# Performance work log

Measured on AMD Instinct MI355X. Metric: run time of the kernel, lower is better.

The kernel has to match this reference:

```python
import jax, jax.numpy as jnp
import numpy as np

C, H, W = 16, 16, 16      # observation_shape
T, B = 128, 128           # rollout steps x num envs
HID = 512                 # LSTM / fc hidden
ZD = 8                    # z_dim (options)
AD = 7                    # action_dim
FE = 128                  # lo_feat dim


def setup_inputs() -> dict:
    key = jax.random.key(0)
    ks = jax.random.split(key, 16)
    def rn(k, shape, s=0.02):
        return jax.random.normal(k, shape, jnp.float32) * s
    return dict(
        x=jax.random.normal(ks[0], (T * B, C, H, W), jnp.float32),
        done=jax.random.randint(ks[1], (T * B,), 0, 2, jnp.int32),
        z=jax.random.randint(ks[2], (T * B,), 0, ZD, jnp.int32),
        action=jax.random.randint(ks[3], (T * B,), 0, AD, jnp.int32),
        h0=jnp.zeros((1, B, HID), jnp.float32),
        c0=jnp.zeros((1, B, HID), jnp.float32),
        conv1_w=rn(ks[4], (C, C, 5, 5)), conv1_b=jnp.zeros((C,), jnp.float32),
        conv2_w=rn(ks[5], (C, C, 3, 3)), conv2_b=jnp.zeros((C,), jnp.float32),
        conv3_w=rn(ks[6], (C, C, 3, 3)), conv3_b=jnp.zeros((C,), jnp.float32),
        fc1_w=rn(ks[7], (HID, C * H * W)), fc1_b=jnp.zeros((HID,), jnp.float32),
        fc2_w=rn(ks[8], (HID, HID)), fc2_b=jnp.zeros((HID,), jnp.float32),
        w_ih=rn(ks[9], (4 * HID, HID)), w_hh=rn(ks[10], (4 * HID, HID)),
        b_ih=jnp.zeros((4 * HID,), jnp.float32), b_hh=jnp.zeros((4 * HID,), jnp.float32),
        lofeat_w=rn(ks[11], (FE, HID + ZD)), lofeat_b=jnp.zeros((FE,), jnp.float32),
        actor_w=rn(ks[12], (AD, FE)), actor_b=jnp.zeros((AD,), jnp.float32),
        critic_w=rn(ks[13], (1, FE)), critic_b=jnp.zeros((1,), jnp.float32),
    )


def _leaky(v):
    return jnp.where(v > 0, v, 0.01 * v)  # nn.LeakyReLU default slope


def reference(x, done, z, action, h0, c0,
              conv1_w, conv1_b, conv2_w, conv2_b, conv3_w, conv3_b,
              fc1_w, fc1_b, fc2_w, fc2_b,
              w_ih, w_hh, b_ih, b_hh,
              lofeat_w, lofeat_b, actor_w, actor_b, critic_w, critic_b):
    dn = ('NCHW', 'OIHW', 'NCHW')
    h = x
    for wgt, bias in ((conv1_w, conv1_b), (conv2_w, conv2_b), (conv3_w, conv3_b)):
        h = _leaky(jax.lax.conv_general_dilated(h, wgt, (1, 1), 'SAME',
                                                dimension_numbers=dn)
                   + bias[None, :, None, None])
    h = h.reshape(h.shape[0], -1)                 # [TB, C*H*W]
    h = _leaky(h @ fc1_w.T + fc1_b)
    h = _leaky(h @ fc2_w.T + fc2_b)               # [TB, 512]

    hs = h.reshape(T, B, HID)                     # env_first=False layout
    ds = done.astype(h.dtype).reshape(T, B)

    def step(carry, inp):
        hc, cc = carry
        xt, dt = inp
        m = (1.0 - dt)[:, None]                   # done-based state reset
        gates = xt @ w_ih.T + b_ih + (hc * m) @ w_hh.T + b_hh
        i, f, g, o = jnp.split(gates, 4, axis=-1)  # PyTorch i,f,g,o order
        c_new = jax.nn.sigmoid(f) * (cc * m) + jax.nn.sigmoid(i) * jnp.tanh(g)
        h_new = jax.nn.sigmoid(o) * jnp.tanh(c_new)
        return (h_new, c_new), h_new

    _, outs = jax.lax.scan(step, (h0[0], c0[0]), (hs, ds))
    feat = outs.reshape(T * B, HID)

    zoh = jax.nn.one_hot(z, ZD, dtype=feat.dtype)
    lf = _leaky(jnp.concatenate([feat, zoh], axis=-1) @ lofeat_w.T + lofeat_b)
    logits = lf @ actor_w.T + actor_b
    logp = jax.nn.log_softmax(logits, axis=-1)
    probs = jnp.exp(logp)
    lp_a = jnp.take_along_axis(logp, action[:, None], axis=-1)[:, 0]
    entropy = -jnp.sum(probs * logp, axis=-1)
    value = lf @ critic_w.T + critic_b            # [TB, 1]
    # pack (log_prob, entropy, value, probs) -> [TB, 3+AD]
    return jnp.concatenate([lp_a[:, None], entropy[:, None], value, probs], axis=-1)
```

## Files before the change

### kernel.cpp

```cpp
#include <hip/hip_runtime.h>
#include <hip/hip_bf16.h>
#include <math.h>

#define TT   128
#define BB   128
#define TB   (TT*BB)
#define CHW  4096
#define HID  512
#define G4   2048
#define ZD   8
#define AD   7
#define FE   128
#define LOFK 520

typedef __attribute__((ext_vector_type(8))) short short8;
typedef __attribute__((ext_vector_type(4))) float f32x4;

__device__ __forceinline__ unsigned short f2b(float f) {
  unsigned int u = __float_as_uint(f);
  unsigned int r = (u + 0x7FFFu + ((u >> 16) & 1u)) >> 16;
  return (unsigned short)r;
}
__device__ __forceinline__ float b2f(unsigned short us) {
  return __uint_as_float(((unsigned int)us) << 16);
}

__device__ __forceinline__ void glds16(const void* g, void* l) {
  __builtin_amdgcn_global_load_lds((const __attribute__((address_space(1))) void*)g,
                                   (__attribute__((address_space(3))) void*)l, 16, 0, 0);
}

__global__ __launch_bounds__(256) void conv_mfma_kernel(
    const float* __restrict__ x,
    const unsigned short* __restrict__ bp1, const unsigned short* __restrict__ bp2,
    const unsigned short* __restrict__ bp3,
    const float* __restrict__ b1, const float* __restrict__ b2, const float* __restrict__ b3,
    unsigned short* __restrict__ out)
{
  __shared__ unsigned short img[2 * 6400];
  const int tid = threadIdx.x;
  const int wv = tid >> 6, lane = tid & 63, quad = lane >> 4, l16 = lane & 15;
  const int imgid = blockIdx.x;
  unsigned short* buf0 = img;
  unsigned short* buf1 = img + 6400;

  {
    int4 z = {0, 0, 0, 0};
    for (int i = tid; i < 1600; i += 256) ((int4*)img)[i] = z;
  }
  __syncthreads();
  const float* src = x + (size_t)imgid * CHW;
  for (int i = tid; i < CHW; i += 256) {
    const int ci = i >> 8, rem = i & 255, y = rem >> 4, xx = rem & 15;
    buf0[(((ci >> 3) * 400) + (y + 2) * 20 + (xx + 2)) * 8 + (ci & 7)] = f2b(src[i]);
  }
  __syncthreads();

  {
    short8 bf[13];
#pragma unroll
    for (int s = 0; s < 13; ++s)
      bf[s] = *(const short8*)(bp1 + l16 * 416 + s * 32 + quad * 8);
    f32x4 acc[4];
#pragma unroll
    for (int mt = 0; mt < 4; ++mt)
#pragma unroll
      for (int r = 0; r < 4; ++r) acc[mt][r] = 0.f;
#pragma unroll
    for (int s = 0; s < 13; ++s) {
      int t = 2 * s + (quad >> 1); if (t > 24) t = 24;
      const int ky = t / 5, kx = t - ky * 5;
      const int base = ((quad & 1) * 400 + ky * 20 + l16 + kx) * 8;
#pragma unroll
      for (int mt = 0; mt < 4; ++mt) {
        const int y = wv * 4 + mt;
        short8 a = *(const short8*)&buf0[base + y * 160];
        acc[mt] = __builtin_amdgcn_mfma_f32_16x16x32_bf16(a, bf[s], acc[mt], 0, 0, 0);
      }
    }
    const float bias = b1[l16];
#pragma unroll
    for (int mt = 0; mt < 4; ++mt) {
      const int y = wv * 4 + mt;
#pragma unroll
      for (int r = 0; r < 4; ++r) {
        float v = acc[mt][r] + bias;
        v = v > 0.f ? v : 0.01f * v;
        const int xx = quad * 4 + r;
        buf1[(((l16 >> 3) * 400) + (y + 2) * 20 + (xx + 2)) * 8 + (l16 & 7)] = f2b(v);
      }
    }
  }
  __syncthreads();

  {
    short8 bf[5];
#pragma unroll
    for (int s = 0; s < 5; ++s)
      bf[s] = *(const short8*)(bp2 + l16 * 160 + s * 32 + quad * 8);
    f32x4 acc[4];
#pragma unroll
    for (int mt = 0; mt < 4; ++mt)
#pragma unroll
      for (int r = 0; r < 4; ++r) acc[mt][r] = 0.f;
#pragma unroll
    for (int s = 0; s < 5; ++s) {
      int t = 2 * s + (quad >> 1); if (t > 8) t = 8;
      const int ky = t / 3, kx = t - ky * 3;
      const int base = ((quad & 1) * 400 + (ky + 1) * 20 + l16 + kx + 1) * 8;
#pragma unroll
      for (int mt = 0; mt < 4; ++mt) {
        const int y = wv * 4 + mt;
        short8 a = *(const short8*)&buf1[base + y * 160];
        acc[mt] = __builtin_amdgcn_mfma_f32_16x16x32_bf16(a, bf[s], acc[mt], 0, 0, 0);
      }
    }
    const float bias = b2[l16];
#pragma unroll
    for (int mt = 0; mt < 4; ++mt) {
      const int y = wv * 4 + mt;
#pragma unroll
      for (int r = 0; r < 4; ++r) {
        float v = acc[mt][r] + bias;
        v = v > 0.f ? v : 0.01f * v;
        const int xx = quad * 4 + r;
        buf0[(((l16 >> 3) * 400) + (y + 2) * 20 + (xx + 2)) * 8 + (l16 & 7)] = f2b(v);
      }
    }
  }
  __syncthreads();

  {
    short8 bf[5];
#pragma unroll
    for (int s = 0; s < 5; ++s)
      bf[s] = *(const short8*)(bp3 + l16 * 160 + s * 32 + quad * 8);
    f32x4 acc[4];
#pragma unroll
    for (int mt = 0; mt < 4; ++mt)
#pragma unroll
      for (int r = 0; r < 4; ++r) acc[mt][r] = 0.f;
#pragma unroll
    for (int s = 0; s < 5; ++s) {
      int t = 2 * s + (quad >> 1); if (t > 8) t = 8;
      const int ky = t / 3, kx = t - ky * 3;
      const int base = ((quad & 1) * 400 + (ky + 1) * 20 + l16 + kx + 1) * 8;
#pragma unroll
      for (int mt = 0; mt < 4; ++mt) {
        const int y = wv * 4 + mt;
        short8 a = *(const short8*)&buf0[base + y * 160];
        acc[mt] = __builtin_amdgcn_mfma_f32_16x16x32_bf16(a, bf[s], acc[mt], 0, 0, 0);
      }
    }
    const float bias = b3[l16];
    unsigned short* dst = out + (size_t)imgid * CHW;
#pragma unroll
    for (int mt = 0; mt < 4; ++mt) {
      const int y = wv * 4 + mt;
      ushort4 pk;
      float v;
      v = acc[mt][0] + bias; v = v > 0.f ? v : 0.01f * v; pk.x = f2b(v);
      v = acc[mt][1] + bias; v = v > 0.f ? v : 0.01f * v; pk.y = f2b(v);
      v = acc[mt][2] + bias; v = v > 0.f ? v : 0.01f * v; pk.z = f2b(v);
      v = acc[mt][3] + bias; v = v > 0.f ? v : 0.01f * v; pk.w = f2b(v);
      *(ushort4*)(dst + l16 * 256 + y * 16 + quad * 4) = pk;
    }
  }
}

__global__ void pack_convw(const float* __restrict__ w, unsigned short* __restrict__ bp,
                           int K, int KH) {
  int i = blockIdx.x * 256 + threadIdx.x;
  if (i >= 16 * K) return;
  int co = i / K, k = i - co * K;
  int t = k >> 4, ci = k & 15;
  float v = 0.f;
  if (t < KH * KH) v = w[((co * 16 + ci) * KH + t / KH) * KH + t % KH];
  bp[i] = f2b(v);
}

template<bool LEAKY, int MODE, int ALAYOUT>
__global__ __launch_bounds__(256) void mfma_fc(
    const unsigned short* __restrict__ A, const unsigned short* __restrict__ W,
    const float* __restrict__ bias, void* __restrict__ outp, int K, int M) {
  __shared__ unsigned short As[128 * 32];
  __shared__ unsigned short Bs[128 * 32];
  const int tid = threadIdx.x;
  const int wv = tid >> 6, lane = tid & 63;
  const int quad = lane >> 4, l16 = lane & 15;
  const int wr = (wv >> 1) * 64, wc = (wv & 1) * 64;
  const int rb = blockIdx.y * 128, cb = blockIdx.x * 128;

  const int s0 = tid, s1 = tid + 256;
  const int r0 = s0 >> 2, q0 = s0 & 3;
  const int r1 = s1 >> 2, q1 = s1 & 3;
  const unsigned short* A0;
  const unsigned short* A1;
  if (ALAYOUT == 0) {
    A0 = A + (size_t)(rb + r0) * K + q0 * 8;
    A1 = A + (size_t)(rb + r1) * K + q1 * 8;
  } else {
    A0 = A + ((size_t)(rb >> 7) * 32 + (q0 >> 1)) * 2048 + (size_t)r0 * 16 + (q0 & 1) * 8;
    A1 = A + ((size_t)(rb >> 7) * 32 + (q1 >> 1)) * 2048 + (size_t)r1 * 16 + (q1 & 1) * 8;
  }
  const unsigned short* W0 = W + (size_t)(cb + r0) * K + q0 * 8;
  const unsigned short* W1 = W + (size_t)(cb + r1) * K + q1 * 8;
  void* ldsA0 = (void*)&As[(wv * 64) * 8];
  void* ldsA1 = (void*)&As[(256 + wv * 64) * 8];
  void* ldsB0 = (void*)&Bs[(wv * 64) * 8];
  void* ldsB1 = (void*)&Bs[(256 + wv * 64) * 8];

  f32x4 acc[4][4];
#pragma unroll
  for (int i = 0; i < 4; ++i)
#pragma unroll
    for (int j = 0; j < 4; ++j)
#pragma unroll
      for (int r = 0; r < 4; ++r) acc[i][j][r] = 0.f;

  for (int k0 = 0; k0 < K; k0 += 32) {
    const int ka = (ALAYOUT == 0) ? k0 : k0 * 128;
    glds16(A0 + ka, ldsA0);
    glds16(A1 + ka, ldsA1);
    glds16(W0 + k0, ldsB0);
    glds16(W1 + k0, ldsB1);
    __syncthreads();
    short8 af[4], bfr[4];
#pragma unroll
    for (int i = 0; i < 4; ++i)
      af[i] = *(const short8*)&As[(wr + i * 16 + l16) * 32 + quad * 8];
#pragma unroll
    for (int j = 0; j < 4; ++j)
      bfr[j] = *(const short8*)&Bs[(wc + j * 16 + l16) * 32 + quad * 8];
#pragma unroll
    for (int i = 0; i < 4; ++i)
#pragma unroll
      for (int j = 0; j < 4; ++j)
        acc[i][j] = __builtin_amdgcn_mfma_f32_16x16x32_bf16(af[i], bfr[j], acc[i][j], 0, 0, 0);
    __syncthreads();
  }

#pragma unroll
  for (int j = 0; j < 4; ++j) {
    const int col = cb + wc + j * 16 + l16;
    const float bj = bias ? bias[col] : 0.f;
#pragma unroll
    for (int i = 0; i < 4; ++i) {
#pragma unroll
      for (int r = 0; r < 4; ++r) {
        const size_t row = rb + wr + i * 16 + quad * 4 + r;
        float v = acc[i][j][r] + bj;
        if (LEAKY) v = v > 0.f ? v : 0.01f * v;
        if (MODE == 0)      ((float*)outp)[row * M + col] = v;
        else if (MODE == 1) ((unsigned short*)outp)[row * M + col] = f2b(v);
        else {
          const size_t idx = row * M + ((size_t)(col & (HID - 1)) * 4 + (col >> 9));
          ((unsigned short*)outp)[idx] = f2b(v);
        }
      }
    }
  }
}

__global__ __launch_bounds__(256, 1) void lstm_persistent(
    const unsigned short* __restrict__ gpk,
    const unsigned short* __restrict__ whh,
    unsigned short* h0m, unsigned short* h1m,
    const float* __restrict__ cm0,
    const int* __restrict__ done,
    unsigned short* __restrict__ feat,
    unsigned int* flags)
{
  __shared__ __align__(16) unsigned short whs[64][520];
  __shared__ __align__(16) unsigned short hpub[128][16];
  __shared__ __align__(16) unsigned short fpub[128][16];
  const int tid = threadIdx.x, wv = tid >> 6, lane = tid & 63;
  const int quad = lane >> 4, l16 = lane & 15;
  const int bid = blockIdx.x;
  const int j0 = bid * 16;
  const int j = j0 + l16;

  for (int rr = wv; rr < 64; rr += 4)
    *(short8*)&whs[rr][lane * 8] =
        *(const short8*)(whh + ((size_t)((rr >> 4) * HID + j0 + (rr & 15))) * HID + lane * 8);

  float creg[2][4], dcur[2][4];
  unsigned long long gcur[2][4], gnxt[2][4];
  int dnxt[2][4];
#pragma unroll
  for (int i = 0; i < 2; ++i)
#pragma unroll
    for (int r = 0; r < 4; ++r) {
      const int b = wv * 32 + i * 16 + quad * 4 + r;
      creg[i][r] = cm0[(size_t)b * HID + j];
      gcur[i][r] = *(const unsigned long long*)(gpk + ((size_t)b * HID + j) * 4);
      dcur[i][r] = 1.f - (float)done[BB + b];
    }
  __syncthreads();

  const int tin = (wv * 32 + l16) * 16 + (quad & 1) * 8;
  const int qb  = (quad >> 1) * 2048;

  for (int t = 0; t < TT; ++t) {
    const unsigned short* hc = (t & 1) ? h1m : h0m;
    unsigned short* hn = (t & 1) ? h0m : h1m;

    if (t + 1 < TT) {
      const unsigned short* gn = gpk + (size_t)(t + 1) * BB * HID * 4;
      const int tn2 = (t + 2 < TT) ? t + 2 : TT - 1;
#pragma unroll
      for (int i = 0; i < 2; ++i)
#pragma unroll
        for (int r = 0; r < 4; ++r) {
          const int b = wv * 32 + i * 16 + quad * 4 + r;
          gnxt[i][r] = *(const unsigned long long*)(gn + ((size_t)b * HID + j) * 4);
          dnxt[i][r] = done[(size_t)tn2 * BB + b];
        }
    }
    asm volatile("" ::: "memory");

    if (t > 0) {
      if (wv == 0) {
        const unsigned int need = (unsigned int)t;
        for (;;) {
          unsigned int v = 0xffffffffu;
          if (lane < 32)
            v = __hip_atomic_load(&flags[lane << 6], __ATOMIC_RELAXED, __HIP_MEMORY_SCOPE_AGENT);
          unsigned long long ok = __ballot(v >= need);
          if (ok == ~0ull) break;
          __builtin_amdgcn_s_sleep(1);
        }
      }
      __syncthreads();
    }

    unsigned long long hq[16][4];
#pragma unroll
    for (int ci = 0; ci < 16; ++ci) {
      const int m = (ci + (bid >> 1) + 1) & 15;
      const unsigned short* base = hc + m * 4096 + qb + tin;
      const unsigned long long* p0 = (const unsigned long long*)base;
      const unsigned long long* p1 = (const unsigned long long*)(base + 256);
      hq[ci][0] = __hip_atomic_load(p0,     __ATOMIC_RELAXED, __HIP_MEMORY_SCOPE_AGENT);
      hq[ci][1] = __hip_atomic_load(p0 + 1, __ATOMIC_RELAXED, __HIP_MEMORY_SCOPE_AGENT);
      hq[ci][2] = __hip_atomic_load(p1,     __ATOMIC_RELAXED, __HIP_MEMORY_SCOPE_AGENT);
      hq[ci][3] = __hip_atomic_load(p1 + 1, __ATOMIC_RELAXED, __HIP_MEMORY_SCOPE_AGENT);
    }
    asm volatile("" ::: "memory");

    f32x4 acc[2][4];
#pragma unroll
    for (int i = 0; i < 2; ++i)
#pragma unroll
      for (int g = 0; g < 4; ++g)
#pragma unroll
        for (int r = 0; r < 4; ++r) acc[i][g][r] = 0.f;

#pragma unroll
    for (int ci = 0; ci < 16; ++ci) {
      const int m = (ci + (bid >> 1) + 1) & 15;
      const int k = m * 32 + quad * 8;
      union { unsigned long long q[2]; short8 v; } a0, a1;
      a0.q[0] = hq[ci][0];
      a0.q[1] = hq[ci][1];
      a1.q[0] = hq[ci][2];
      a1.q[1] = hq[ci][3];
      short8 b0 = *(const short8*)&whs[l16][k];
      short8 b1 = *(const short8*)&whs[16 + l16][k];
      short8 b2 = *(const short8*)&whs[32 + l16][k];
      short8 b3 = *(const short8*)&whs[48 + l16][k];
      acc[0][0] = __builtin_amdgcn_mfma_f32_16x16x32_bf16(a0.v, b0, acc[0][0], 0, 0, 0);
      acc[0][1] = __builtin_amdgcn_mfma_f32_16x16x32_bf16(a0.v, b1, acc[0][1], 0, 0, 0);
      acc[0][2] = __builtin_amdgcn_mfma_f32_16x16x32_bf16(a0.v, b2, acc[0][2], 0, 0, 0);
      acc[0][3] = __builtin_amdgcn_mfma_f32_16x16x32_bf16(a0.v, b3, acc[0][3], 0, 0, 0);
      acc[1][0] = __builtin_amdgcn_mfma_f32_16x16x32_bf16(a1.v, b0, acc[1][0], 0, 0, 0);
      acc[1][1] = __builtin_amdgcn_mfma_f32_16x16x32_bf16(a1.v, b1, acc[1][1], 0, 0, 0);
      acc[1][2] = __builtin_amdgcn_mfma_f32_16x16x32_bf16(a1.v, b2, acc[1][2], 0, 0, 0);
      acc[1][3] = __builtin_amdgcn_mfma_f32_16x16x32_bf16(a1.v, b3, acc[1][3], 0, 0, 0);
    }

#pragma unroll
    for (int i = 0; i < 2; ++i) {
#pragma unroll
      for (int r = 0; r < 4; ++r) {
        const int b = wv * 32 + i * 16 + quad * 4 + r;
        const unsigned long long gq = gcur[i][r];
        const float gi = acc[i][0][r] + b2f((unsigned short)gq);
        const float gf = acc[i][1][r] + b2f((unsigned short)(gq >> 16));
        const float gg = acc[i][2][r] + b2f((unsigned short)(gq >> 32));
        const float go = acc[i][3][r] + b2f((unsigned short)(gq >> 48));
        const float i_s = 1.f / (1.f + __expf(-gi));
        const float f_s = 1.f / (1.f + __expf(-gf));
        const float o_s = 1.f / (1.f + __expf(-go));
        const float g_t = tanhf(gg);
        const float c_new = f_s * creg[i][r] + i_s * g_t;
        const float h_new = o_s * tanhf(c_new);
        const float mn = dcur[i][r];
        creg[i][r] = c_new * mn;
        hpub[b][l16] = f2b(h_new * mn);
        fpub[b][l16] = f2b(h_new);
      }
    }
    __syncthreads();

    if (t < TT - 1) {
      const unsigned long long* hp = (const unsigned long long*)hpub;
      unsigned long long* d = (unsigned long long*)(hn + bid * 2048 + tid * 8);
      __hip_atomic_store(d,     hp[tid * 2],     __ATOMIC_RELAXED, __HIP_MEMORY_SCOPE_AGENT);
      __hip_atomic_store(d + 1, hp[tid * 2 + 1], __ATOMIC_RELAXED, __HIP_MEMORY_SCOPE_AGENT);
      asm volatile("s_waitcnt vmcnt(0)" ::: "memory");
    }
    __syncthreads();
    if (t < TT - 1 && tid == 0)
      __hip_atomic_store(&flags[bid << 6], (unsigned int)(t + 1),
                         __ATOMIC_RELAXED, __HIP_MEMORY_SCOPE_AGENT);

    *(int4*)(feat + ((size_t)t * 32 + bid) * 2048 + tid * 8) = ((const int4*)fpub)[tid];

#pragma unroll
    for (int i = 0; i < 2; ++i)
#pragma unroll
      for (int r = 0; r < 4; ++r) {
        gcur[i][r] = gnxt[i][r];
        dcur[i][r] = 1.f - (float)dnxt[i][r];
      }
  }
}

__global__ void f2b_kernel(const float* __restrict__ in, unsigned short* __restrict__ out, int n) {
  int i = blockIdx.x * 256 + threadIdx.x;
  if (i < n) out[i] = f2b(in[i]);
}
__global__ void lofpack_kernel(const float* __restrict__ lw, unsigned short* __restrict__ out) {
  int i = blockIdx.x * 256 + threadIdx.x;
  int r = i >> 9, c = i & 511;
  out[i] = f2b(lw[r * LOFK + c]);
}
__global__ void bias_add_kernel(const float* __restrict__ a, const float* __restrict__ b,
                                float* __restrict__ o, int n) {
  int i = blockIdx.x * 256 + threadIdx.x;
  if (i < n) o[i] = a[i] + b[i];
}
__global__ void lstm_init_kernel(const float* __restrict__ h0, const float* __restrict__ c0,
                                 const int* __restrict__ done0,
                                 unsigned short* __restrict__ hm, float* __restrict__ cmp) {
  int i = blockIdx.x * 256 + threadIdx.x;
  int env = i >> 9, col = i & 511;
  float m = 1.f - (float)done0[env];
  hm[(col >> 4) * 2048 + env * 16 + (col & 15)] = f2b(h0[i] * m);
  cmp[i] = c0[i] * m;
}

__global__ __launch_bounds__(256) void heads_kernel(
    const float* __restrict__ raw, const float* __restrict__ lw, const float* __restrict__ lb,
    const float* __restrict__ aw, const float* __restrict__ ab,
    const float* __restrict__ cw, const float* __restrict__ cbias,
    const int* __restrict__ z, const int* __restrict__ action,
    float* __restrict__ out) {
  const int lane = threadIdx.x & 63;
  const int s = blockIdx.x * 4 + (threadIdx.x >> 6);
  const int zv = z[s];
  float v0 = raw[(size_t)s * FE + lane]      + lw[(size_t)lane * LOFK + HID + zv]        + lb[lane];
  float v1 = raw[(size_t)s * FE + 64 + lane] + lw[(size_t)(64 + lane) * LOFK + HID + zv] + lb[64 + lane];
  v0 = v0 > 0.f ? v0 : 0.01f * v0;
  v1 = v1 > 0.f ? v1 : 0.01f * v1;

  float logits[AD];
#pragma unroll
  for (int jj = 0; jj < AD; ++jj) {
    float p = aw[jj * FE + lane] * v0 + aw[jj * FE + 64 + lane] * v1;
#pragma unroll
    for (int o = 32; o > 0; o >>= 1) p += __shfl_down(p, o, 64);
    logits[jj] = __shfl(p, 0, 64) + ab[jj];
  }
  float val = cw[lane] * v0 + cw[64 + lane] * v1;
#pragma unroll
  for (int o = 32; o > 0; o >>= 1) val += __shfl_down(val, o, 64);
  val = __shfl(val, 0, 64) + cbias[0];

  float mx = logits[0];
#pragma unroll
  for (int jj = 1; jj < AD; ++jj) mx = fmaxf(mx, logits[jj]);
  float ex[AD], S = 0.f;
#pragma unroll
  for (int jj = 0; jj < AD; ++jj) { ex[jj] = __expf(logits[jj] - mx); S += ex[jj]; }
  const float inv = 1.f / S;
  const float lZ = __logf(S) + mx;
  float ent = 0.f;
#pragma unroll
  for (int jj = 0; jj < AD; ++jj) ent += (ex[jj] * inv) * (logits[jj] - lZ);
  ent = -ent;
  const float lp_a = logits[action[s]] - lZ;

  if (lane < 10) {
    float v;
    if (lane == 0)      v = lp_a;
    else if (lane == 1) v = ent;
    else if (lane == 2) v = val;
    else                v = ex[lane - 3] * inv;
    out[(size_t)s * 10 + lane] = v;
  }
}

extern "C" void kernel_launch(void* const* d_in, const int* in_sizes, int n_in,
                              void* d_out, int out_size, void* d_ws, size_t ws_size,
                              hipStream_t stream) {
  const float* x       = (const float*)d_in[0];
  const int*   done    = (const int*)d_in[1];
  const int*   z       = (const int*)d_in[2];
  const int*   action  = (const int*)d_in[3];
  const float* h0      = (const float*)d_in[4];
  const float* c0      = (const float*)d_in[5];
  const float* conv1_w = (const float*)d_in[6];
  const float* conv1_b = (const float*)d_in[7];
  const float* conv2_w = (const float*)d_in[8];
  const float* conv2_b = (const float*)d_in[9];
  const float* conv3_w = (const float*)d_in[10];
  const float* conv3_b = (const float*)d_in[11];
  const float* fc1_w   = (const float*)d_in[12];
  const float* fc1_b   = (const float*)d_in[13];
  const float* fc2_w   = (const float*)d_in[14];
  const float* fc2_b   = (const float*)d_in[15];
  const float* w_ih    = (const float*)d_in[16];
  const float* w_hh    = (const float*)d_in[17];
  const float* b_ih    = (const float*)d_in[18];
  const float* b_hh    = (const float*)d_in[19];
  const float* lofeat_w= (const float*)d_in[20];
  const float* lofeat_b= (const float*)d_in[21];
  const float* actor_w = (const float*)d_in[22];
  const float* actor_b = (const float*)d_in[23];
  const float* critic_w= (const float*)d_in[24];
  const float* critic_b= (const float*)d_in[25];
  float* out = (float*)d_out;

  char* p = (char*)d_ws;
  unsigned short* conv3out = (unsigned short*)p;
  unsigned short* gatesP   = (unsigned short*)p;
  p += (size_t)TB * CHW * 2;
  unsigned short* fc1out   = (unsigned short*)p;   p += (size_t)TB * HID * 2;
  unsigned short* fc2out   = (unsigned short*)p;   p += (size_t)TB * HID * 2;
  unsigned short* feat     = (unsigned short*)p;   p += (size_t)TB * HID * 2;
  float*          rawlf    = (float*)p;            p += (size_t)TB * FE * 4;
  unsigned short* fc1w_bf  = (unsigned short*)p;   p += (size_t)HID * CHW * 2;
  unsigned short* fc2w_bf  = (unsigned short*)p;   p += (size_t)HID * HID * 2;
  unsigned short* wih_bf   = (unsigned short*)p;   p += (size_t)G4 * HID * 2;
  unsigned short* whh_bf   = (unsigned short*)p;   p += (size_t)G4 * HID * 2;
  unsigned short* lofw_bf  = (unsigned short*)p;   p += (size_t)FE * HID * 2;
  unsigned short* bp1      = (unsigned short*)p;   p += 16 * 416 * 2;
  unsigned short* bp2      = (unsigned short*)p;   p += 16 * 160 * 2;
  unsigned short* bp3      = (unsigned short*)p;   p += 16 * 160 * 2;
  float*          combbias = (float*)p;            p += (size_t)G4 * 4;
  unsigned short* hmA      = (unsigned short*)p;   p += (size_t)BB * HID * 2;
  unsigned short* hmB      = (unsigned short*)p;   p += (size_t)BB * HID * 2;
  float*          cm       = (float*)p;            p += (size_t)BB * HID * 4;
  unsigned int*   flags    = (unsigned int*)p;     p += 32 * 64 * 4;

  hipMemsetAsync(flags, 0, 32 * 64 * 4, stream);
  pack_convw<<<26, 256, 0, stream>>>(conv1_w, bp1, 416, 5);
  pack_convw<<<10, 256, 0, stream>>>(conv2_w, bp2, 160, 3);
  pack_convw<<<10, 256, 0, stream>>>(conv3_w, bp3, 160, 3);
  f2b_kernel<<<(HID * CHW + 255) / 256, 256, 0, stream>>>(fc1_w, fc1w_bf, HID * CHW);
  f2b_kernel<<<(HID * HID + 255) / 256, 256, 0, stream>>>(fc2_w, fc2w_bf, HID * HID);
  f2b_kernel<<<(G4 * HID + 255) / 256, 256, 0, stream>>>(w_ih, wih_bf, G4 * HID);
  f2b_kernel<<<(G4 * HID + 255) / 256, 256, 0, stream>>>(w_hh, whh_bf, G4 * HID);
  lofpack_kernel<<<(FE * HID + 255) / 256, 256, 0, stream>>>(lofeat_w, lofw_bf);
  bias_add_kernel<<<(G4 + 255) / 256, 256, 0, stream>>>(b_ih, b_hh, combbias, G4);
  lstm_init_kernel<<<(BB * HID + 255) / 256, 256, 0, stream>>>(h0, c0, done, hmA, cm);
  conv_mfma_kernel<<<TB, 256, 0, stream>>>(x, bp1, bp2, bp3,
                                           conv1_b, conv2_b, conv3_b, conv3out);
  mfma_fc<true, 1, 0><<<dim3(HID / 128, TB / 128), 256, 0, stream>>>(
      conv3out, fc1w_bf, fc1_b, fc1out, CHW, HID);
  mfma_fc<true, 1, 0><<<dim3(HID / 128, TB / 128), 256, 0, stream>>>(
      fc1out, fc2w_bf, fc2_b, fc2out, HID, HID);
  mfma_fc<false, 2, 0><<<dim3(G4 / 128, TB / 128), 256, 0, stream>>>(
      fc2out, wih_bf, combbias, gatesP, HID, G4);
  lstm_persistent<<<32, 256, 0, stream>>>(gatesP, whh_bf, hmA, hmB, cm, done, feat, flags);
  mfma_fc<false, 0, 1><<<dim3(FE / 128, TB / 128), 256, 0, stream>>>(
      feat, lofw_bf, nullptr, rawlf, HID, FE);
  heads_kernel<<<TB / 4, 256, 0, stream>>>(rawlf, lofeat_w, lofeat_b, actor_w, actor_b,
                                           critic_w, critic_b, z, action, out);
}
```

Before: 1.633 ms.

## Repartition persistent LSTM across 128 blocks with register-resident W_hh and env groups

The recurrent LSTM kernel now runs on 128 blocks instead of 32. Each block owns 16 environments and a 32-column hidden slice, so it only waits on the 16 blocks in its environment group rather than on all blocks. W_hh fragments are kept in registers instead of LDS, and gate results are exchanged through a small shared buffer. The hidden-state and feat layouts change to a group-tiled format, and the downstream GEMM's A-addressing and the init kernel are updated to match. This spreads the sequential critical path across more CUs and reduces global sync fan-in. In exchange it raises register pressure and adds an extra LDS round-trip and barrier per step.

```diff
diff --git a/kernel.cpp b/kernel.cpp
--- a/kernel.cpp
+++ b/kernel.cpp
@@ -200,8 +200,8 @@
     A0 = A + (size_t)(rb + r0) * K + q0 * 8;
     A1 = A + (size_t)(rb + r1) * K + q1 * 8;
   } else {
-    A0 = A + ((size_t)(rb >> 7) * 32 + (q0 >> 1)) * 2048 + (size_t)r0 * 16 + (q0 & 1) * 8;
-    A1 = A + ((size_t)(rb >> 7) * 32 + (q1 >> 1)) * 2048 + (size_t)r1 * 16 + (q1 & 1) * 8;
+    A0 = A + (size_t)(rb >> 7) * 65536 + (r0 >> 4) * 8192 + (r0 & 15) * 32 + q0 * 8;
+    A1 = A + (size_t)(rb >> 7) * 65536 + (r1 >> 4) * 8192 + (r1 & 15) * 32 + q1 * 8;
   }
   const unsigned short* W0 = W + (size_t)(cb + r0) * K + q0 * 8;
   const unsigned short* W1 = W + (size_t)(cb + r1) * K + q1 * 8;
@@ -219,7 +219,7 @@
       for (int r = 0; r < 4; ++r) acc[i][j][r] = 0.f;
 
   for (int k0 = 0; k0 < K; k0 += 32) {
-    const int ka = (ALAYOUT == 0) ? k0 : k0 * 128;
+    const int ka = (ALAYOUT == 0) ? k0 : k0 * 16;
     glds16(A0 + ka, ldsA0);
     glds16(A1 + ka, ldsA1);
     glds16(W0 + k0, ldsB0);
@@ -271,35 +271,35 @@
     unsigned short* __restrict__ feat,
     unsigned int* flags)
 {
-  __shared__ __align__(16) unsigned short whs[64][520];
-  __shared__ __align__(16) unsigned short hpub[128][16];
-  __shared__ __align__(16) unsigned short fpub[128][16];
+  __shared__ __align__(16) float gl[4 * 528 + 8];
+  __shared__ __align__(16) unsigned short hpub[16 * 32];
+  __shared__ __align__(16) unsigned short fpub[16 * 32];
   const int tid = threadIdx.x, wv = tid >> 6, lane = tid & 63;
   const int quad = lane >> 4, l16 = lane & 15;
   const int bid = blockIdx.x;
-  const int j0 = bid * 16;
-  const int j = j0 + l16;
-
-  for (int rr = wv; rr < 64; rr += 4)
-    *(short8*)&whs[rr][lane * 8] =
-        *(const short8*)(whh + ((size_t)((rr >> 4) * HID + j0 + (rr & 15))) * HID + lane * 8);
-
-  float creg[2][4], dcur[2][4];
-  unsigned long long gcur[2][4], gnxt[2][4];
-  int dnxt[2][4];
-#pragma unroll
-  for (int i = 0; i < 2; ++i)
-#pragma unroll
-    for (int r = 0; r < 4; ++r) {
-      const int b = wv * 32 + i * 16 + quad * 4 + r;
-      creg[i][r] = cm0[(size_t)b * HID + j];
-      gcur[i][r] = *(const unsigned long long*)(gpk + ((size_t)b * HID + j) * 4);
-      dcur[i][r] = 1.f - (float)done[BB + b];
-    }
-  __syncthreads();
-
-  const int tin = (wv * 32 + l16) * 16 + (quad & 1) * 8;
-  const int qb  = (quad >> 1) * 2048;
+  const int g = bid & 7, s = bid >> 3;
+  const int j0 = s * 32;
+
+  short8 wfrag[2][16];
+#pragma unroll
+  for (int jt = 0; jt < 2; ++jt)
+#pragma unroll
+    for (int ci = 0; ci < 16; ++ci)
+      wfrag[jt][ci] = *(const short8*)(whh +
+          (size_t)(wv * HID + j0 + jt * 16 + l16) * HID + ci * 32 + quad * 8);
+
+  const int env_t = tid >> 4;
+  const int jA = (tid & 15) * 2;
+  const int eg = g * 16 + env_t;
+  float creg[2], dcur;
+  unsigned long long gcur[2], gnxt[2];
+  int dnxt = 0;
+  creg[0] = cm0[(size_t)eg * HID + j0 + jA];
+  creg[1] = cm0[(size_t)eg * HID + j0 + jA + 1];
+  gcur[0] = *(const unsigned long long*)(gpk + ((size_t)eg * HID + j0 + jA) * 4);
+  gcur[1] = *(const unsigned long long*)(gpk + ((size_t)eg * HID + j0 + jA + 1) * 4);
+  dcur = 1.f - (float)done[BB + eg];
+  gnxt[0] = gcur[0]; gnxt[1] = gcur[1];
 
   for (int t = 0; t < TT; ++t) {
     const unsigned short* hc = (t & 1) ? h1m : h0m;
@@ -307,15 +307,10 @@
 
     if (t + 1 < TT) {
       const unsigned short* gn = gpk + (size_t)(t + 1) * BB * HID * 4;
+      gnxt[0] = *(const unsigned long long*)(gn + ((size_t)eg * HID + j0 + jA) * 4);
+      gnxt[1] = *(const unsigned long long*)(gn + ((size_t)eg * HID + j0 + jA + 1) * 4);
       const int tn2 = (t + 2 < TT) ? t + 2 : TT - 1;
-#pragma unroll
-      for (int i = 0; i < 2; ++i)
-#pragma unroll
-        for (int r = 0; r < 4; ++r) {
-          const int b = wv * 32 + i * 16 + quad * 4 + r;
-          gnxt[i][r] = *(const unsigned long long*)(gn + ((size_t)b * HID + j) * 4);
-          dnxt[i][r] = done[(size_t)tn2 * BB + b];
-        }
+      dnxt = done[(size_t)tn2 * BB + eg];
     }
     asm volatile("" ::: "memory");
 
@@ -324,8 +319,9 @@
         const unsigned int need = (unsigned int)t;
         for (;;) {
           unsigned int v = 0xffffffffu;
-          if (lane < 32)
-            v = __hip_atomic_load(&flags[lane << 6], __ATOMIC_RELAXED, __HIP_MEMORY_SCOPE_AGENT);
+          if (lane < 16)
+            v = __hip_atomic_load(&flags[((lane << 3) | g) << 6],
+                                  __ATOMIC_RELAXED, __HIP_MEMORY_SCOPE_AGENT);
           unsigned long long ok = __ballot(v >= need);
           if (ok == ~0ull) break;
           __builtin_amdgcn_s_sleep(1);
@@ -334,96 +330,82 @@
       __syncthreads();
     }
 
-    unsigned long long hq[16][4];
+    unsigned long long hq[16][2];
 #pragma unroll
     for (int ci = 0; ci < 16; ++ci) {
-      const int m = (ci + (bid >> 1) + 1) & 15;
-      const unsigned short* base = hc + m * 4096 + qb + tin;
-      const unsigned long long* p0 = (const unsigned long long*)base;
-      const unsigned long long* p1 = (const unsigned long long*)(base + 256);
-      hq[ci][0] = __hip_atomic_load(p0,     __ATOMIC_RELAXED, __HIP_MEMORY_SCOPE_AGENT);
-      hq[ci][1] = __hip_atomic_load(p0 + 1, __ATOMIC_RELAXED, __HIP_MEMORY_SCOPE_AGENT);
-      hq[ci][2] = __hip_atomic_load(p1,     __ATOMIC_RELAXED, __HIP_MEMORY_SCOPE_AGENT);
-      hq[ci][3] = __hip_atomic_load(p1 + 1, __ATOMIC_RELAXED, __HIP_MEMORY_SCOPE_AGENT);
+      const unsigned long long* p =
+          (const unsigned long long*)(hc + g * 8192 + ci * 512 + l16 * 32 + quad * 8);
+      hq[ci][0] = __hip_atomic_load(p,     __ATOMIC_RELAXED, __HIP_MEMORY_SCOPE_AGENT);
+      hq[ci][1] = __hip_atomic_load(p + 1, __ATOMIC_RELAXED, __HIP_MEMORY_SCOPE_AGENT);
     }
     asm volatile("" ::: "memory");
 
-    f32x4 acc[2][4];
-#pragma unroll
-    for (int i = 0; i < 2; ++i)
-#pragma unroll
-      for (int g = 0; g < 4; ++g)
-#pragma unroll
-        for (int r = 0; r < 4; ++r) acc[i][g][r] = 0.f;
+    f32x4 acc[2];
+#pragma unroll
+    for (int jt = 0; jt < 2; ++jt)
+#pragma unroll
+      for (int r = 0; r < 4; ++r) acc[jt][r] = 0.f;
 
 #pragma unroll
     for (int ci = 0; ci < 16; ++ci) {
-      const int m = (ci + (bid >> 1) + 1) & 15;
-      const int k = m * 32 + quad * 8;
-      union { unsigned long long q[2]; short8 v; } a0, a1;
-      a0.q[0] = hq[ci][0];
-      a0.q[1] = hq[ci][1];
-      a1.q[0] = hq[ci][2];
-      a1.q[1] = hq[ci][3];
-      short8 b0 = *(const short8*)&whs[l16][k];
-      short8 b1 = *(const short8*)&whs[16 + l16][k];
-      short8 b2 = *(const short8*)&whs[32 + l16][k];
-      short8 b3 = *(const short8*)&whs[48 + l16][k];
-      acc[0][0] = __builtin_amdgcn_mfma_f32_16x16x32_bf16(a0.v, b0, acc[0][0], 0, 0, 0);
-      acc[0][1] = __builtin_amdgcn_mfma_f32_16x16x32_bf16(a0.v, b1, acc[0][1], 0, 0, 0);
-      acc[0][2] = __builtin_amdgcn_mfma_f32_16x16x32_bf16(a0.v, b2, acc[0][2], 0, 0, 0);
-      acc[0][3] = __builtin_amdgcn_mfma_f32_16x16x32_bf16(a0.v, b3, acc[0][3], 0, 0, 0);
-      acc[1][0] = __builtin_amdgcn_mfma_f32_16x16x32_bf16(a1.v, b0, acc[1][0], 0, 0, 0);
-      acc[1][1] = __builtin_amdgcn_mfma_f32_16x16x32_bf16(a1.v, b1, acc[1][1], 0, 0, 0);
-      acc[1][2] = __builtin_amdgcn_mfma_f32_16x16x32_bf16(a1.v, b2, acc[1][2], 0, 0, 0);
-      acc[1][3] = __builtin_amdgcn_mfma_f32_16x16x32_bf16(a1.v, b3, acc[1][3], 0, 0, 0);
-    }
-
-#pragma unroll
-    for (int i = 0; i < 2; ++i) {
-#pragma unroll
-      for (int r = 0; r < 4; ++r) {
-        const int b = wv * 32 + i * 16 + quad * 4 + r;
-        const unsigned long long gq = gcur[i][r];
-        const float gi = acc[i][0][r] + b2f((unsigned short)gq);
-        const float gf = acc[i][1][r] + b2f((unsigned short)(gq >> 16));
-        const float gg = acc[i][2][r] + b2f((unsigned short)(gq >> 32));
-        const float go = acc[i][3][r] + b2f((unsigned short)(gq >> 48));
+      union { unsigned long long q[2]; short8 v; } a;
+      a.q[0] = hq[ci][0];
+      a.q[1] = hq[ci][1];
+      acc[0] = __builtin_amdgcn_mfma_f32_16x16x32_bf16(a.v, wfrag[0][ci], acc[0], 0, 0, 0);
+      acc[1] = __builtin_amdgcn_mfma_f32_16x16x32_bf16(a.v, wfrag[1][ci], acc[1], 0, 0, 0);
+    }
+
+#pragma unroll
+    for (int jt = 0; jt < 2; ++jt)
+#pragma unroll
+      for (int r = 0; r < 4; ++r)
+        gl[wv * 528 + (quad * 4 + r) * 33 + jt * 16 + l16] = acc[jt][r];
+    __syncthreads();
+
+    {
+      unsigned int hw = 0, fw = 0;
+#pragma unroll
+      for (int pp = 0; pp < 2; ++pp) {
+        const int jj = jA + pp;
+        const unsigned long long gq = gcur[pp];
+        const float gi = gl[0 * 528 + env_t * 33 + jj] + b2f((unsigned short)gq);
+        const float gf = gl[1 * 528 + env_t * 33 + jj] + b2f((unsigned short)(gq >> 16));
+        const float gg = gl[2 * 528 + env_t * 33 + jj] + b2f((unsigned short)(gq >> 32));
+        const float go = gl[3 * 528 + env_t * 33 + jj] + b2f((unsigned short)(gq >> 48));
         const float i_s = 1.f / (1.f + __expf(-gi));
         const float f_s = 1.f / (1.f + __expf(-gf));
         const float o_s = 1.f / (1.f + __expf(-go));
         const float g_t = tanhf(gg);
-        const float c_new = f_s * creg[i][r] + i_s * g_t;
+        const float c_new = f_s * creg[pp] + i_s * g_t;
         const float h_new = o_s * tanhf(c_new);
-        const float mn = dcur[i][r];
-        creg[i][r] = c_new * mn;
-        hpub[b][l16] = f2b(h_new * mn);
-        fpub[b][l16] = f2b(h_new);
-      }
+        creg[pp] = c_new * dcur;
+        hw |= (unsigned int)f2b(h_new * dcur) << (16 * pp);
+        fw |= (unsigned int)f2b(h_new) << (16 * pp);
+      }
+      *(unsigned int*)&hpub[env_t * 32 + jA] = hw;
+      *(unsigned int*)&fpub[env_t * 32 + jA] = fw;
     }
     __syncthreads();
 
-    if (t < TT - 1) {
+    if (t < TT - 1 && tid < 64) {
       const unsigned long long* hp = (const unsigned long long*)hpub;
-      unsigned long long* d = (unsigned long long*)(hn + bid * 2048 + tid * 8);
+      unsigned long long* d = (unsigned long long*)(hn + g * 8192 + s * 512 + tid * 8);
       __hip_atomic_store(d,     hp[tid * 2],     __ATOMIC_RELAXED, __HIP_MEMORY_SCOPE_AGENT);
       __hip_atomic_store(d + 1, hp[tid * 2 + 1], __ATOMIC_RELAXED, __HIP_MEMORY_SCOPE_AGENT);
-      asm volatile("s_waitcnt vmcnt(0)" ::: "memory");
-    }
+    }
+    asm volatile("s_waitcnt vmcnt(0)" ::: "memory");
     __syncthreads();
     if (t < TT - 1 && tid == 0)
       __hip_atomic_store(&flags[bid << 6], (unsigned int)(t + 1),
                          __ATOMIC_RELAXED, __HIP_MEMORY_SCOPE_AGENT);
 
-    *(int4*)(feat + ((size_t)t * 32 + bid) * 2048 + tid * 8) = ((const int4*)fpub)[tid];
-
-#pragma unroll
-    for (int i = 0; i < 2; ++i)
-#pragma unroll
-      for (int r = 0; r < 4; ++r) {
-        gcur[i][r] = gnxt[i][r];
-        dcur[i][r] = 1.f - (float)dnxt[i][r];
-      }
+    if (tid < 64)
+      *(int4*)(feat + (size_t)t * 65536 + g * 8192 + s * 512 + tid * 8) =
+          ((const int4*)fpub)[tid];
+
+    gcur[0] = gnxt[0];
+    gcur[1] = gnxt[1];
+    dcur = 1.f - (float)dnxt;
   }
 }
 
@@ -447,7 +429,7 @@
   int i = blockIdx.x * 256 + threadIdx.x;
   int env = i >> 9, col = i & 511;
   float m = 1.f - (float)done0[env];
-  hm[(col >> 4) * 2048 + env * 16 + (col & 15)] = f2b(h0[i] * m);
+  hm[(env >> 4) * 8192 + (col >> 5) * 512 + (env & 15) * 32 + (col & 31)] = f2b(h0[i] * m);
   cmp[i] = c0[i] * m;
 }
 
@@ -553,9 +535,9 @@
   unsigned short* hmA      = (unsigned short*)p;   p += (size_t)BB * HID * 2;
   unsigned short* hmB      = (unsigned short*)p;   p += (size_t)BB * HID * 2;
   float*          cm       = (float*)p;            p += (size_t)BB * HID * 4;
-  unsigned int*   flags    = (unsigned int*)p;     p += 32 * 64 * 4;
-
-  hipMemsetAsync(flags, 0, 32 * 64 * 4, stream);
+  unsigned int*   flags    = (unsigned int*)p;     p += 128 * 64 * 4;
+
+  hipMemsetAsync(flags, 0, 128 * 64 * 4, stream);
   pack_convw<<<26, 256, 0, stream>>>(conv1_w, bp1, 416, 5);
   pack_convw<<<10, 256, 0, stream>>>(conv2_w, bp2, 160, 3);
   pack_convw<<<10, 256, 0, stream>>>(conv3_w, bp3, 160, 3);
@@ -574,7 +556,7 @@
       fc1out, fc2w_bf, fc2_b, fc2out, HID, HID);
   mfma_fc<false, 2, 0><<<dim3(G4 / 128, TB / 128), 256, 0, stream>>>(
       fc2out, wih_bf, combbias, gatesP, HID, G4);
-  lstm_persistent<<<32, 256, 0, stream>>>(gatesP, whh_bf, hmA, hmB, cm, done, feat, flags);
+  lstm_persistent<<<128, 256, 0, stream>>>(gatesP, whh_bf, hmA, hmB, cm, done, feat, flags);
   mfma_fc<false, 0, 1><<<dim3(FE / 128, TB / 128), 256, 0, stream>>>(
       feat, lofw_bf, nullptr, rawlf, HID, FE);
   heads_kernel<<<TB / 4, 256, 0, stream>>>(rawlf, lofeat_w, lofeat_b, actor_w, actor_b,
```

New measurement: 1.380 ms. 15.5% less time.
